# Kernel tuning notes

Hardware: AMD Instinct MI355X
Metric: run time of the kernel (lower is better)

Reference implementation:

```python
import jax, jax.numpy as jnp
import numpy as np

C = 1024
HEADS = 8
HD = C // HEADS
SF = 2
EPS = 1e-6
N, D, H, W = 2, 32, 40, 32


def _ln(x, w, b):
    m = jnp.mean(x, -1, keepdims=True)
    v = jnp.mean((x - m) ** 2, -1, keepdims=True)
    return (x - m) * jax.lax.rsqrt(v + EPS) * w + b


def _mlp2(x, w1, b1, w2, b2):
    # Linear -> exact GELU -> Linear (matches nn.Sequential(Linear, GELU, Linear))
    return jax.nn.gelu(x @ w1.T + b1, approximate=False) @ w2.T + b2


def setup_inputs() -> dict:
    key = jax.random.key(0)
    ks = jax.random.split(key, 24)
    p = lambda i, shape: jax.random.normal(ks[i], shape, jnp.float32) * 0.02
    return {
        "x": jax.random.normal(ks[0], (N, D, H, W, C), jnp.float32),
        "q_w": p(1, (C, C)),
        "k_w1": p(2, (C, C)), "k_b1": p(3, (C,)),
        "k_w2": p(4, (C, C)), "k_b2": p(5, (C,)),
        "v_w1": p(6, (C, C)), "v_b1": p(7, (C,)),
        "v_w2": p(8, (C, C)), "v_b2": p(9, (C,)),
        "lnq_w": jnp.ones((C,), jnp.float32), "lnq_b": jnp.zeros((C,), jnp.float32),
        "lnk_w": jnp.ones((C,), jnp.float32), "lnk_b": jnp.zeros((C,), jnp.float32),
        "lnv_w": jnp.ones((C,), jnp.float32), "lnv_b": jnp.zeros((C,), jnp.float32),
        "in_w": p(10, (3 * C, C)), "in_b": p(11, (3 * C,)),
        "out_w": p(12, (C, C)), "out_b": p(13, (C,)),
        "mlp_w1": p(14, (2 * C, C)), "mlp_b1": p(15, (2 * C,)),
        "mlp_w2": p(16, (2 * C, 2 * C)), "mlp_b2": p(17, (2 * C,)),
    }


def reference(x, q_w, k_w1, k_b1, k_w2, k_b2, v_w1, v_b1, v_w2, v_b2,
              lnq_w, lnq_b, lnk_w, lnk_b, lnv_w, lnv_b,
              in_w, in_b, out_w, out_b, mlp_w1, mlp_b1, mlp_w2, mlp_b2):
    n, d, h, w, c = x.shape
    dg, hg, wg = d // SF, h // SF, w // SF
    cube = SF ** 3

    x_flat = x.reshape(n, -1, c)                      # [N, T, C], T = D*H*W
    k = _ln(_mlp2(x_flat, k_w1, k_b1, k_w2, k_b2), lnk_w, lnk_b)
    v = _ln(_mlp2(x_flat, v_w1, v_b1, v_w2, v_b2), lnv_w, lnv_b)

    # Trilinear downsample by exactly 2 (align_corners=False) == 2x2x2 mean pool.
    q = x.reshape(n, dg, SF, hg, SF, wg, SF, c).mean(axis=(2, 4, 6))
    q = q.reshape(n, -1, c)                            # [N, Q, C]
    query = _ln(q @ q_w.T, lnq_w, lnq_b)               # q_proj_1 has no bias

    def regions(t):
        t = t.reshape(n, dg, SF, hg, SF, wg, SF, c)
        t = t.transpose(0, 1, 3, 5, 2, 4, 6, 7)
        return t.reshape(n, dg * hg * wg, cube, c)     # [N, Q, 8, C]

    k_r = regions(k)
    v_r = regions(v)

    wq, wk, wv = in_w[:C], in_w[C:2 * C], in_w[2 * C:]
    bq, bk, bv = in_b[:C], in_b[C:2 * C], in_b[2 * C:]
    qh = (query @ wq.T + bq).reshape(n, -1, HEADS, HD)           # [N,Q,h,hd]
    kh = (k_r @ wk.T + bk).reshape(n, -1, cube, HEADS, HD)       # [N,Q,8,h,hd]
    vh = (v_r @ wv.T + bv).reshape(n, -1, cube, HEADS, HD)

    scale = 1.0 / np.sqrt(HD).astype(np.float32)
    scores = jnp.einsum('nqhd,nqkhd->nqhk', qh, kh) * scale
    attn = jax.nn.softmax(scores, axis=-1)
    o = jnp.einsum('nqhk,nqkhd->nqhd', attn, vh).reshape(n, -1, c)
    o = o @ out_w.T + out_b                            # MHA out_proj

    o = _mlp2(o, mlp_w1, mlp_b1, mlp_w2, mlp_b2)       # [N, Q, 2C]
    return o.reshape(n, dg, hg, wg, 2 * c)
```

## Files before the change

### kernel.cpp

```cpp
#include <hip/hip_runtime.h>

typedef __attribute__((ext_vector_type(8))) short bf16x8;
typedef __attribute__((ext_vector_type(4))) float f32x4;
typedef unsigned short u16;

__device__ inline u16 f2b(float f) {
  union { float f; unsigned u; } x; x.f = f;
  unsigned r = x.u + 0x7FFFu + ((x.u >> 16) & 1u);
  return (u16)(r >> 16);
}
__device__ inline float b2f(u16 s) {
  union { unsigned u; float f; } x; x.u = ((unsigned)s) << 16;
  return x.f;
}
__device__ inline float gelu_f(float v) {
  return 0.5f * v * (1.0f + erff(v * 0.70710678118654752f));
}
__device__ inline void gll16(const void* g, void* lds) {
  __builtin_amdgcn_global_load_lds((const __attribute__((address_space(1))) void*)g,
                                   (__attribute__((address_space(3))) void*)lds,
                                   16, 0, 0);
}

__global__ __launch_bounds__(256) void cvt_w(const float* __restrict__ s,
                                             u16* __restrict__ d, int n4) {
  int i = blockIdx.x * 256 + threadIdx.x;
  if (i < n4) {
    float4 v = ((const float4*)s)[i];
    ushort4 o; o.x = f2b(v.x); o.y = f2b(v.y); o.z = f2b(v.z); o.w = f2b(v.w);
    ((ushort4*)d)[i] = o;
  }
}

__global__ __launch_bounds__(256) void cat_bias(const float* __restrict__ a,
                                                const float* __restrict__ b,
                                                float* __restrict__ o) {
  int i = blockIdx.x * 256 + threadIdx.x;
  if (i < 1024) { o[i] = a[i]; o[1024 + i] = b[i]; }
}

__global__ __launch_bounds__(256) void pool_cvt(const float* __restrict__ xg,
                                                u16* __restrict__ Xb,
                                                u16* __restrict__ Qp) {
  int qr = blockIdx.x;
  int wgi = qr & 15;
  int hgi = (qr >> 4) % 20;
  int dgi = qr / 320;
  int c = threadIdx.x * 4;
  float sx = 0.f, sy = 0.f, sz = 0.f, sw = 0.f;
#pragma unroll
  for (int j = 0; j < 8; ++j) {
    int tr = ((2 * dgi + (j >> 2)) * 40 + (2 * hgi + ((j >> 1) & 1))) * 32 +
             (2 * wgi + (j & 1));
    long off = (long)tr * 1024 + c;
    float4 v = *(const float4*)&xg[off];
    ushort4 o; o.x = f2b(v.x); o.y = f2b(v.y); o.z = f2b(v.z); o.w = f2b(v.w);
    *(ushort4*)&Xb[off] = o;
    sx += v.x; sy += v.y; sz += v.z; sw += v.w;
  }
  ushort4 o;
  o.x = f2b(sx * 0.125f); o.y = f2b(sy * 0.125f);
  o.z = f2b(sz * 0.125f); o.w = f2b(sw * 0.125f);
  *(ushort4*)&Qp[(long)qr * 1024 + c] = o;
}

__global__ __launch_bounds__(256) void ln_ip(u16* __restrict__ X,
                                             const float* __restrict__ w,
                                             const float* __restrict__ b) {
  long row = blockIdx.x;
  int c = threadIdx.x * 4;
  ushort4 v = *(const ushort4*)&X[row * 1024 + c];
  float f0 = b2f(v.x), f1 = b2f(v.y), f2 = b2f(v.z), f3 = b2f(v.w);
  float s = f0 + f1 + f2 + f3;
  float q = f0 * f0 + f1 * f1 + f2 * f2 + f3 * f3;
#pragma unroll
  for (int off = 32; off >= 1; off >>= 1) {
    s += __shfl_xor(s, off);
    q += __shfl_xor(q, off);
  }
  __shared__ float red[8];
  int wv = threadIdx.x >> 6, ln = threadIdx.x & 63;
  if (ln == 0) { red[wv] = s; red[4 + wv] = q; }
  __syncthreads();
  s = red[0] + red[1] + red[2] + red[3];
  q = red[4] + red[5] + red[6] + red[7];
  float mean = s * (1.f / 1024.f);
  float var = q * (1.f / 1024.f) - mean * mean;
  float rs = rsqrtf(var + 1e-6f);
  float4 wv4 = *(const float4*)&w[c];
  float4 bv4 = *(const float4*)&b[c];
  ushort4 o;
  o.x = f2b((f0 - mean) * rs * wv4.x + bv4.x);
  o.y = f2b((f1 - mean) * rs * wv4.y + bv4.y);
  o.z = f2b((f2 - mean) * rs * wv4.z + bv4.z);
  o.w = f2b((f3 - mean) * rs * wv4.w + bv4.w);
  *(ushort4*)&X[row * 1024 + c] = o;
}

__global__ __launch_bounds__(256) void ln2_ip(u16* X1, const float* w1,
                                              const float* b1, u16* X2,
                                              const float* w2, const float* b2,
                                              long rows1) {
  long row = blockIdx.x;
  u16* X = X1; const float* w = w1; const float* b = b1;
  if (row >= rows1) { X = X2; w = w2; b = b2; row -= rows1; }
  int c = threadIdx.x * 4;
  ushort4 v = *(const ushort4*)&X[row * 1024 + c];
  float f0 = b2f(v.x), f1 = b2f(v.y), f2 = b2f(v.z), f3 = b2f(v.w);
  float s = f0 + f1 + f2 + f3;
  float q = f0 * f0 + f1 * f1 + f2 * f2 + f3 * f3;
#pragma unroll
  for (int off = 32; off >= 1; off >>= 1) {
    s += __shfl_xor(s, off);
    q += __shfl_xor(q, off);
  }
  __shared__ float red[8];
  int wv = threadIdx.x >> 6, ln = threadIdx.x & 63;
  if (ln == 0) { red[wv] = s; red[4 + wv] = q; }
  __syncthreads();
  s = red[0] + red[1] + red[2] + red[3];
  q = red[4] + red[5] + red[6] + red[7];
  float mean = s * (1.f / 1024.f);
  float var = q * (1.f / 1024.f) - mean * mean;
  float rs = rsqrtf(var + 1e-6f);
  float4 wv4 = *(const float4*)&w[c];
  float4 bv4 = *(const float4*)&b[c];
  ushort4 o;
  o.x = f2b((f0 - mean) * rs * wv4.x + bv4.x);
  o.y = f2b((f1 - mean) * rs * wv4.y + bv4.y);
  o.z = f2b((f2 - mean) * rs * wv4.z + bv4.z);
  o.w = f2b((f3 - mean) * rs * wv4.w + bv4.w);
  *(ushort4*)&X[row * 1024 + c] = o;
}

#define MFMA16(a, b, c) __builtin_amdgcn_mfma_f32_16x16x32_bf16((a), (b), (c), 0, 0, 0)

#define BK 32
template <int EPI, int KT>
__global__ __launch_bounds__(256, 4) void gemm_bt(const u16* A, const u16* B,
                                                  const float* bias,
                                                  float* __restrict__ Cf, u16* Cb,
                                                  int M1, int N, int lda,
                                                  int nbx, int nby,
                                                  const u16* A2, const u16* B2,
                                                  const float* bias2, u16* Cb2, int M2,
                                                  const u16* A3, const u16* B3,
                                                  const float* bias3, u16* Cb3, int M3) {
  __shared__ __align__(16) u16 As0[128 * BK];
  __shared__ __align__(16) u16 Bs0[128 * BK];
  __shared__ __align__(16) u16 As1[128 * BK];
  __shared__ __align__(16) u16 Bs1[128 * BK];
  const int tid = threadIdx.x;

  int L = blockIdx.x, bx, by;
  if ((nbx & 7) == 0) {
    int xcd = L & 7, j = L >> 3, ppx = nbx >> 3;
    int pj = j / nby;
    bx = xcd * ppx + pj;
    by = j - pj * nby;
  } else {
    bx = L % nbx;
    by = L / nbx;
  }
  int bm = bx * 128;
  const int bn = by * 128;

  int M = M1;
  if (bm >= M1) {
    if (bm < M1 + M2) { A = A2; B = B2; bias = bias2; Cb = Cb2; bm -= M1; M = M2; }
    else { A = A3; B = B3; bias = bias3; Cb = Cb3; bm -= (M1 + M2); M = M3; }
  }

  const int l = tid & 63, wv = tid >> 6;
  const int wm = (wv >> 1) * 64, wn = (wv & 1) * 64;
  const int lr = l & 15, kg = l >> 4;

  const int q0 = tid, q1 = 256 + tid;
  const int r0 = q0 >> 2, r1 = q1 >> 2;
  const int ca = ((q0 & 3) ^ ((r0 >> 1) & 3)) * 8;
  const int cbn = ((q1 & 3) ^ ((r1 >> 1) & 3)) * 8;
  const int ea = q0 * 8, eb = q1 * 8;
  int gra = bm + r0; if (gra > M - 1) gra = M - 1;
  int grb = bm + r1; if (grb > M - 1) grb = M - 1;
  const u16* pa0 = A + (long)gra * lda + ca;
  const u16* pa1 = A + (long)grb * lda + cbn;
  const u16* pb0 = B + (long)(bn + r0) * KT + ca;
  const u16* pb1 = B + (long)(bn + r1) * KT + cbn;

  const int swz = (kg ^ ((lr >> 1) & 3)) * 8;

  f32x4 acc[4][4] = {};
  const int nt = KT / BK;

#define STAGE(AS, BS, k0)                \
  do {                                   \
    gll16(pa0 + (k0), &(AS)[ea]);        \
    gll16(pb0 + (k0), &(BS)[ea]);        \
    gll16(pa1 + (k0), &(AS)[eb]);        \
    gll16(pb1 + (k0), &(BS)[eb]);        \
  } while (0)

#define COMPUTE(AS, BS)                                                       \
  do {                                                                        \
    bf16x8 af[4], bfr[4];                                                     \
    _Pragma("unroll") for (int m = 0; m < 4; ++m)                             \
        af[m] = *(const bf16x8*)&(AS)[(wm + m * 16 + lr) * BK + swz];         \
    _Pragma("unroll") for (int n = 0; n < 4; ++n)                             \
        bfr[n] = *(const bf16x8*)&(BS)[(wn + n * 16 + lr) * BK + swz];        \
    _Pragma("unroll") for (int m = 0; m < 4; ++m)                             \
        _Pragma("unroll") for (int n = 0; n < 4; ++n)                         \
            acc[m][n] = MFMA16(af[m], bfr[n], acc[m][n]);                     \
  } while (0)

  STAGE(As0, Bs0, 0);
  __syncthreads();
#pragma unroll
  for (int t = 0; t < nt; t += 2) {
    if (t + 1 < nt) STAGE(As1, Bs1, (t + 1) * BK);
    COMPUTE(As0, Bs0);
    __syncthreads();
    if (t + 2 < nt) STAGE(As0, Bs0, (t + 2) * BK);
    COMPUTE(As1, Bs1);
    __syncthreads();
  }
#undef STAGE
#undef COMPUTE

#pragma unroll
  for (int m = 0; m < 4; ++m) {
    int row0 = bm + wm + m * 16 + kg * 4;
#pragma unroll
    for (int n = 0; n < 4; ++n) {
      int col = bn + wn + n * 16 + lr;
      float bsv = (EPI == 3) ? 0.f : bias[col];
#pragma unroll
      for (int r = 0; r < 4; ++r) {
        int row = row0 + r;
        if (row < M) {
          float v = acc[m][n][r] + bsv;
          if (EPI == 1) v = gelu_f(v);
          if (EPI == 2) Cf[(long)row * N + col] = v;
          else Cb[(long)row * N + col] = f2b(v);
        }
      }
    }
  }
}

__global__ __launch_bounds__(256) void attn_k(const u16* __restrict__ QH,
                                              const u16* __restrict__ KH,
                                              const u16* __restrict__ VH,
                                              u16* __restrict__ O) {
  int qr = blockIdx.x;
  int wgi = qr & 15;
  int hgi = (qr >> 4) % 20;
  int dgi = qr / 320;
  int c0 = (threadIdx.x >> 5) * 128 + (threadIdx.x & 31) * 4;
  ushort4 qv = *(const ushort4*)&QH[(long)qr * 1024 + c0];
  float q0 = b2f(qv.x), q1 = b2f(qv.y), q2 = b2f(qv.z), q3 = b2f(qv.w);
  long trs[8];
  float sc[8];
#pragma unroll
  for (int j = 0; j < 8; ++j) {
    int tr = ((2 * dgi + (j >> 2)) * 40 + (2 * hgi + ((j >> 1) & 1))) * 32 +
             (2 * wgi + (j & 1));
    trs[j] = (long)tr * 1024 + c0;
    ushort4 kv = *(const ushort4*)&KH[trs[j]];
    float p = q0 * b2f(kv.x) + q1 * b2f(kv.y) + q2 * b2f(kv.z) + q3 * b2f(kv.w);
    p += __shfl_xor(p, 16); p += __shfl_xor(p, 8); p += __shfl_xor(p, 4);
    p += __shfl_xor(p, 2);  p += __shfl_xor(p, 1);
    sc[j] = p * 0.088388347648318447f;
  }
  float mx = sc[0];
#pragma unroll
  for (int j = 1; j < 8; ++j) mx = fmaxf(mx, sc[j]);
  float ssum = 0.f;
#pragma unroll
  for (int j = 0; j < 8; ++j) { sc[j] = expf(sc[j] - mx); ssum += sc[j]; }
  float inv = 1.0f / ssum;
  float o0 = 0, o1 = 0, o2 = 0, o3 = 0;
#pragma unroll
  for (int j = 0; j < 8; ++j) {
    ushort4 vv = *(const ushort4*)&VH[trs[j]];
    float p = sc[j] * inv;
    o0 += p * b2f(vv.x); o1 += p * b2f(vv.y);
    o2 += p * b2f(vv.z); o3 += p * b2f(vv.w);
  }
  ushort4 ov; ov.x = f2b(o0); ov.y = f2b(o1); ov.z = f2b(o2); ov.w = f2b(o3);
  *(ushort4*)&O[(long)qr * 1024 + c0] = ov;
}

extern "C" void kernel_launch(void* const* d_in, const int* in_sizes, int n_in,
                              void* d_out, int out_size, void* d_ws,
                              size_t ws_size, hipStream_t stream) {
  const float* x      = (const float*)d_in[0];
  const float* q_w    = (const float*)d_in[1];
  const float* k_w1   = (const float*)d_in[2];
  const float* k_b1   = (const float*)d_in[3];
  const float* k_w2   = (const float*)d_in[4];
  const float* k_b2   = (const float*)d_in[5];
  const float* v_w1   = (const float*)d_in[6];
  const float* v_b1   = (const float*)d_in[7];
  const float* v_w2   = (const float*)d_in[8];
  const float* v_b2   = (const float*)d_in[9];
  const float* lnq_w  = (const float*)d_in[10];
  const float* lnq_b  = (const float*)d_in[11];
  const float* lnk_w  = (const float*)d_in[12];
  const float* lnk_b  = (const float*)d_in[13];
  const float* lnv_w  = (const float*)d_in[14];
  const float* lnv_b  = (const float*)d_in[15];
  const float* in_w   = (const float*)d_in[16];
  const float* in_b   = (const float*)d_in[17];
  const float* out_w  = (const float*)d_in[18];
  const float* out_b  = (const float*)d_in[19];
  const float* mlp_w1 = (const float*)d_in[20];
  const float* mlp_b1 = (const float*)d_in[21];
  const float* mlp_w2 = (const float*)d_in[22];
  const float* mlp_b2 = (const float*)d_in[23];
  float* out = (float*)d_out;

  char* base = (char*)d_ws;
  size_t off = 0;
  auto alloc_us = [&](size_t elems) -> u16* {
    u16* r = (u16*)(base + off);
    off += ((elems * 2 + 255) & ~(size_t)255);
    return r;
  };
  const size_t CC = 1024 * 1024;
  u16* wb_q   = alloc_us(CC);
  u16* wb_kv1 = alloc_us(2 * CC);
  u16* wb_k2  = alloc_us(CC);
  u16* wb_v2  = alloc_us(CC);
  u16* wb_in  = alloc_us(3 * CC);
  u16* wb_out = alloc_us(CC);
  u16* wb_m1  = alloc_us(2 * CC);
  u16* wb_m2  = alloc_us(4 * CC);
  float* b_kv1 = (float*)(base + off); off += 2048 * 4;

  auto cvt = [&](const float* s, u16* d, size_t n) {
    int n4 = (int)(n / 4);
    cvt_w<<<(n4 + 255) / 256, 256, 0, stream>>>(s, d, n4);
  };
  cvt(q_w, wb_q, CC);
  cvt(k_w1, wb_kv1, CC);        cvt(v_w1, wb_kv1 + CC, CC);
  cvt(k_w2, wb_k2, CC);         cvt(v_w2, wb_v2, CC);
  cvt(in_w, wb_in, 3 * CC);     cvt(out_w, wb_out, CC);
  cvt(mlp_w1, wb_m1, 2 * CC);   cvt(mlp_w2, wb_m2, 4 * CC);
  cat_bias<<<4, 256, 0, stream>>>(k_b1, v_b1, b_kv1);

  int dgc = 1;
  for (int cand = 32; cand >= 1; cand >>= 1) {
    size_t Tc_ = (size_t)cand * 2560;
    if (off + Tc_ * 11520ull + (1ull << 20) <= ws_size) { dgc = cand; break; }
  }
  const int Tc = dgc * 2560;
  const int Tq = dgc * 320;

  u16* Xb  = alloc_us((size_t)Tc * 1024);
  u16* Hb2 = alloc_us((size_t)Tc * 2048);
  u16* Kb  = alloc_us((size_t)Tc * 1024);
  u16* Vb  = alloc_us((size_t)Tc * 1024);
  u16* Qp  = alloc_us((size_t)Tq * 1024);
  u16* QQ  = alloc_us((size_t)Tq * 1024);
  u16* QHb = alloc_us((size_t)Tq * 1024);
  u16* Ob  = alloc_us((size_t)Tq * 1024);
  u16* O2  = alloc_us((size_t)Tq * 1024);
  u16* Hm  = Kb;

  auto launch = [&](int EPI, int N, int K, int lda,
                    const u16* A1, const u16* B1, const float* s1, u16* C1, int M1,
                    const u16* A2, const u16* B2, const float* s2, u16* C2, int M2,
                    const u16* A3, const u16* B3, const float* s3, u16* C3, int M3,
                    float* Cf) {
    int nbx = (M1 + M2 + M3) / 128, nby = N / 128;
    dim3 g(nbx * nby);
    if (K == 1024) {
      switch (EPI) {
        case 0: gemm_bt<0, 1024><<<g, 256, 0, stream>>>(A1, B1, s1, Cf, C1, M1, N, lda, nbx, nby, A2, B2, s2, C2, M2, A3, B3, s3, C3, M3); break;
        case 1: gemm_bt<1, 1024><<<g, 256, 0, stream>>>(A1, B1, s1, Cf, C1, M1, N, lda, nbx, nby, A2, B2, s2, C2, M2, A3, B3, s3, C3, M3); break;
        case 2: gemm_bt<2, 1024><<<g, 256, 0, stream>>>(A1, B1, s1, Cf, C1, M1, N, lda, nbx, nby, A2, B2, s2, C2, M2, A3, B3, s3, C3, M3); break;
        default: gemm_bt<3, 1024><<<g, 256, 0, stream>>>(A1, B1, s1, Cf, C1, M1, N, lda, nbx, nby, A2, B2, s2, C2, M2, A3, B3, s3, C3, M3); break;
      }
    } else {
      switch (EPI) {
        case 0: gemm_bt<0, 2048><<<g, 256, 0, stream>>>(A1, B1, s1, Cf, C1, M1, N, lda, nbx, nby, A2, B2, s2, C2, M2, A3, B3, s3, C3, M3); break;
        case 1: gemm_bt<1, 2048><<<g, 256, 0, stream>>>(A1, B1, s1, Cf, C1, M1, N, lda, nbx, nby, A2, B2, s2, C2, M2, A3, B3, s3, C3, M3); break;
        case 2: gemm_bt<2, 2048><<<g, 256, 0, stream>>>(A1, B1, s1, Cf, C1, M1, N, lda, nbx, nby, A2, B2, s2, C2, M2, A3, B3, s3, C3, M3); break;
        default: gemm_bt<3, 2048><<<g, 256, 0, stream>>>(A1, B1, s1, Cf, C1, M1, N, lda, nbx, nby, A2, B2, s2, C2, M2, A3, B3, s3, C3, M3); break;
      }
    }
  };
  const u16* Z = nullptr;

  for (int dg0 = 0; dg0 < 32; dg0 += dgc) {
    const float* xg = x + (size_t)dg0 * 2560 * 1024;
    long q0g = (long)dg0 * 320;

    pool_cvt<<<Tq, 256, 0, stream>>>(xg, Xb, Qp);

    launch(1, 2048, 1024, 1024, Xb, wb_kv1, b_kv1, Hb2, Tc,
           Z, Z, nullptr, nullptr, 0, Z, Z, nullptr, nullptr, 0, nullptr);

    launch(0, 1024, 1024, 2048, Hb2, wb_k2, k_b2, Kb, Tc,
           Hb2 + 1024, wb_v2, v_b2, Vb, Tc, Z, Z, nullptr, nullptr, 0, nullptr);

    ln2_ip<<<2 * Tc, 256, 0, stream>>>(Kb, lnk_w, lnk_b, Vb, lnv_w, lnv_b, Tc);

    launch(3, 1024, 1024, 1024, Qp, wb_q, nullptr, QQ, Tq,
           Z, Z, nullptr, nullptr, 0, Z, Z, nullptr, nullptr, 0, nullptr);
    ln_ip<<<Tq, 256, 0, stream>>>(QQ, lnq_w, lnq_b);

    launch(0, 1024, 1024, 1024, Kb, wb_in + CC, in_b + 1024, Xb, Tc,
           Vb, wb_in + 2 * CC, in_b + 2048, Hb2, Tc,
           QQ, wb_in, in_b, QHb, Tq, nullptr);

    attn_k<<<Tq, 256, 0, stream>>>(QHb, Xb, Hb2, Ob);

    launch(0, 1024, 1024, 1024, Ob, wb_out, out_b, O2, Tq,
           Z, Z, nullptr, nullptr, 0, Z, Z, nullptr, nullptr, 0, nullptr);
    launch(1, 2048, 1024, 1024, O2, wb_m1, mlp_b1, Hm, Tq,
           Z, Z, nullptr, nullptr, 0, Z, Z, nullptr, nullptr, 0, nullptr);
    launch(2, 2048, 2048, 2048, Hm, wb_m2, mlp_b2, nullptr, Tq,
           Z, Z, nullptr, nullptr, 0, Z, Z, nullptr, nullptr, 0,
           out + q0g * 2048);
  }
}
```

Baseline: 2.250 ms.

## Triple-buffer GEMM LDS staging with manual waitcnt and single barrier per step

Replaces the double-buffered LDS pipeline in the bf16 GEMM with a three-stage ring buffer. Loads are issued two tiles ahead, and each iteration uses a partial vmcnt wait plus one barrier instead of a full __syncthreads after every compute. The aim is to hide global-to-LDS latency better and cut barrier stalls. In exchange, LDS use per block rises by half and the occupancy hint drops from 4 to 3 blocks. The hand-written waitcnt depends on exactly four outstanding loads per stage.

Result: slower. 2.569 ms (+14.2%).

```diff
diff --git a/kernel.cpp b/kernel.cpp
--- a/kernel.cpp
+++ b/kernel.cpp
@@ -137,7 +137,7 @@
 
 #define BK 32
 template <int EPI, int KT>
-__global__ __launch_bounds__(256, 4) void gemm_bt(const u16* A, const u16* B,
+__global__ __launch_bounds__(256, 3) void gemm_bt(const u16* A, const u16* B,
                                                   const float* bias,
                                                   float* __restrict__ Cf, u16* Cb,
                                                   int M1, int N, int lda,
@@ -146,10 +146,7 @@
                                                   const float* bias2, u16* Cb2, int M2,
                                                   const u16* A3, const u16* B3,
                                                   const float* bias3, u16* Cb3, int M3) {
-  __shared__ __align__(16) u16 As0[128 * BK];
-  __shared__ __align__(16) u16 Bs0[128 * BK];
-  __shared__ __align__(16) u16 As1[128 * BK];
-  __shared__ __align__(16) u16 Bs1[128 * BK];
+  __shared__ __align__(16) u16 S[3][2][128 * BK];
   const int tid = threadIdx.x;
 
   int L = blockIdx.x, bx, by;
@@ -192,36 +189,37 @@
   f32x4 acc[4][4] = {};
   const int nt = KT / BK;
 
-#define STAGE(AS, BS, k0)                \
-  do {                                   \
-    gll16(pa0 + (k0), &(AS)[ea]);        \
-    gll16(pb0 + (k0), &(BS)[ea]);        \
-    gll16(pa1 + (k0), &(AS)[eb]);        \
-    gll16(pb1 + (k0), &(BS)[eb]);        \
+#define STAGE(s, k0)                       \
+  do {                                     \
+    gll16(pa0 + (k0), &S[s][0][ea]);       \
+    gll16(pb0 + (k0), &S[s][1][ea]);       \
+    gll16(pa1 + (k0), &S[s][0][eb]);       \
+    gll16(pb1 + (k0), &S[s][1][eb]);       \
   } while (0)
 
-#define COMPUTE(AS, BS)                                                       \
+#define COMPUTE(s)                                                            \
   do {                                                                        \
     bf16x8 af[4], bfr[4];                                                     \
     _Pragma("unroll") for (int m = 0; m < 4; ++m)                             \
-        af[m] = *(const bf16x8*)&(AS)[(wm + m * 16 + lr) * BK + swz];         \
+        af[m] = *(const bf16x8*)&S[s][0][(wm + m * 16 + lr) * BK + swz];      \
     _Pragma("unroll") for (int n = 0; n < 4; ++n)                             \
-        bfr[n] = *(const bf16x8*)&(BS)[(wn + n * 16 + lr) * BK + swz];        \
+        bfr[n] = *(const bf16x8*)&S[s][1][(wn + n * 16 + lr) * BK + swz];     \
     _Pragma("unroll") for (int m = 0; m < 4; ++m)                             \
         _Pragma("unroll") for (int n = 0; n < 4; ++n)                         \
             acc[m][n] = MFMA16(af[m], bfr[n], acc[m][n]);                     \
   } while (0)
 
-  STAGE(As0, Bs0, 0);
-  __syncthreads();
-#pragma unroll
-  for (int t = 0; t < nt; t += 2) {
-    if (t + 1 < nt) STAGE(As1, Bs1, (t + 1) * BK);
-    COMPUTE(As0, Bs0);
-    __syncthreads();
-    if (t + 2 < nt) STAGE(As0, Bs0, (t + 2) * BK);
-    COMPUTE(As1, Bs1);
-    __syncthreads();
+  STAGE(0, 0);
+  STAGE(1, BK);
+#pragma unroll
+  for (int t = 0; t < nt; ++t) {
+    if (t + 1 < nt)
+      asm volatile("s_waitcnt vmcnt(4) lgkmcnt(0)" ::: "memory");
+    else
+      asm volatile("s_waitcnt vmcnt(0) lgkmcnt(0)" ::: "memory");
+    asm volatile("s_barrier" ::: "memory");
+    if (t + 2 < nt) STAGE((t + 2) % 3, (t + 2) * BK);
+    COMPUTE(t % 3);
   }
 #undef STAGE
 #undef COMPUTE
```
